# Kernel tuning notes

Measured on AMD Instinct MI355X. Metric: run time of the kernel, lower is better.

Reference implementation:

```python
import jax, jax.numpy as jnp
import numpy as np

CONTEXT_SIZE = 2048
CONTEXT_DIM = 1024
HIDDEN_SIZE = 1024
BATCH = 32
SEQLEN = 64


def setup_inputs() -> dict:
    key = jax.random.key(0)
    k1, k2, k3 = jax.random.split(key, 3)
    hidden = jax.random.normal(k1, (1, BATCH, HIDDEN_SIZE), dtype=jnp.float32)
    contextvects = jax.random.normal(k2, (CONTEXT_SIZE, BATCH, CONTEXT_DIM), dtype=jnp.float32)
    # nn.Linear weight: [out_features=context_dim, in_features=hidden_size]
    W = jax.random.normal(k3, (CONTEXT_DIM, HIDDEN_SIZE), dtype=jnp.float32) / np.sqrt(HIDDEN_SIZE)
    padding_mask = jnp.zeros((CONTEXT_SIZE, BATCH), dtype=bool)
    return {"seqlen": SEQLEN, "hidden": hidden, "contextvects": contextvects,
            "W": W, "padding_mask": padding_mask}


def reference(seqlen, hidden, contextvects, W, padding_mask):
    # hidden: [1, B, H] -> [B, H]
    h = hidden[0]
    # Linear projection (no bias): [B, D]
    hidden_proj = h @ W.T
    # scores over context positions: [C, B]
    scores = jnp.einsum('cbd,bd->cb', contextvects, hidden_proj)
    scores = jnp.where(padding_mask, -jnp.inf, scores)
    # softmax over context dim (dim=0)
    attn_weights = jax.nn.softmax(scores, axis=0)  # [C, B]
    # weighted sum of context vectors: [B, D]
    ctx = jnp.einsum('cb,cbd->bd', attn_weights, contextvects)
    # the torch loop recomputes identical values for every step -> broadcast
    context = jnp.broadcast_to(ctx[None], (seqlen, ctx.shape[0], ctx.shape[1]))
    attentions = jnp.broadcast_to(attn_weights.T[None],
                                  (seqlen, attn_weights.shape[1], attn_weights.shape[0]))
    return context, attentions
```

## Files before the change

kernel.cpp:

```cpp
#include <hip/hip_runtime.h>
#include <math.h>

#define C_SIZE 2048
#define D_DIM  1024
#define H_DIM  1024
#define B_SIZE 32
#define S_LEN  64
#define G_NUM  32
#define CG     (C_SIZE / G_NUM)

__global__ __launch_bounds__(256) void hp_kernel(const float* __restrict__ hidden,
                                                 const float* __restrict__ W,
                                                 float* __restrict__ hp) {
    int b     = blockIdx.x;
    int dbase = blockIdx.y * 128;
    int lane  = threadIdx.x & 63;
    int wave  = threadIdx.x >> 6;

    const float* hrow = hidden + b * H_DIM;
    float4 h4[4];
#pragma unroll
    for (int k = 0; k < 4; ++k) h4[k] = *(const float4*)(hrow + k * 256 + 4 * lane);

    for (int i = 0; i < 32; ++i) {
        int d = dbase + wave * 32 + i;
        const float* wrow = W + (size_t)d * H_DIM;
        float s = 0.f;
#pragma unroll
        for (int k = 0; k < 4; ++k) {
            float4 w4 = *(const float4*)(wrow + k * 256 + 4 * lane);
            s += w4.x * h4[k].x + w4.y * h4[k].y + w4.z * h4[k].z + w4.w * h4[k].w;
        }
        for (int off = 32; off > 0; off >>= 1) s += __shfl_xor(s, off);
        if (lane == 0) hp[b * D_DIM + d] = s;
    }
}

__global__ __launch_bounds__(256) void fused_kernel(const float* __restrict__ cv,
                                                    const float* __restrict__ hp,
                                                    const unsigned char* __restrict__ mask,
                                                    float* __restrict__ scoresT,
                                                    float* __restrict__ pm,
                                                    float* __restrict__ pl,
                                                    float* __restrict__ pacc) {
    int g    = blockIdx.x;
    int b    = blockIdx.y;
    int lane = threadIdx.x & 63;
    int wave = threadIdx.x >> 6;

    const float* hpb = hp + b * D_DIM;
    float4 hp4[4];
#pragma unroll
    for (int k = 0; k < 4; ++k) hp4[k] = *(const float4*)(hpb + k * 256 + 4 * lane);

    float  m = -3.0e38f, l = 0.f;
    float4 acc[4];
#pragma unroll
    for (int k = 0; k < 4; ++k) acc[k] = make_float4(0.f, 0.f, 0.f, 0.f);

    const int    c0      = g * CG + wave * (CG / 4);
    const size_t cstride = (size_t)B_SIZE * D_DIM;
    const float* p0      = cv + ((size_t)c0 * B_SIZE + b) * D_DIM + 4 * lane;

    float4 nxt[4];
#pragma unroll
    for (int k = 0; k < 4; ++k) nxt[k] = *(const float4*)(p0 + k * 256);

    for (int i = 0; i < 16; ++i) {
        float4 cvv[4];
#pragma unroll
        for (int k = 0; k < 4; ++k) cvv[k] = nxt[k];
        if (i < 15) {
            const float* pn = p0 + (size_t)(i + 1) * cstride;
#pragma unroll
            for (int k = 0; k < 4; ++k) nxt[k] = *(const float4*)(pn + k * 256);
        }
        float s = 0.f;
#pragma unroll
        for (int k = 0; k < 4; ++k) {
            s += cvv[k].x * hp4[k].x + cvv[k].y * hp4[k].y +
                 cvv[k].z * hp4[k].z + cvv[k].w * hp4[k].w;
        }
        for (int off = 32; off > 0; off >>= 1) s += __shfl_xor(s, off);

        int c = c0 + i;
        if (mask[c * B_SIZE + b]) s = -3.0e38f;
        if (lane == 0) scoresT[b * C_SIZE + c] = s;

        if (s <= m) {
            float p = __expf(s - m);
            l += p;
#pragma unroll
            for (int k = 0; k < 4; ++k) {
                acc[k].x += p * cvv[k].x;
                acc[k].y += p * cvv[k].y;
                acc[k].z += p * cvv[k].z;
                acc[k].w += p * cvv[k].w;
            }
        } else {
            float scale = __expf(m - s);
            l = l * scale + 1.f;
#pragma unroll
            for (int k = 0; k < 4; ++k) {
                acc[k].x = acc[k].x * scale + cvv[k].x;
                acc[k].y = acc[k].y * scale + cvv[k].y;
                acc[k].z = acc[k].z * scale + cvv[k].z;
                acc[k].w = acc[k].w * scale + cvv[k].w;
            }
            m = s;
        }
    }

    __shared__ float sm[4], sl[4];
    __shared__ float accs[4][D_DIM];
    if (lane == 0) { sm[wave] = m; sl[wave] = l; }
    __syncthreads();

    float mb = fmaxf(fmaxf(sm[0], sm[1]), fmaxf(sm[2], sm[3]));
    float myscale = __expf(m - mb);
#pragma unroll
    for (int k = 0; k < 4; ++k) {
        float4 v = acc[k];
        v.x *= myscale; v.y *= myscale; v.z *= myscale; v.w *= myscale;
        *(float4*)&accs[wave][k * 256 + 4 * lane] = v;
    }
    float lb = 0.f;
#pragma unroll
    for (int w = 0; w < 4; ++w) lb += sl[w] * __expf(sm[w] - mb);
    __syncthreads();

    int t = threadIdx.x;
    float4 r = make_float4(0.f, 0.f, 0.f, 0.f);
#pragma unroll
    for (int w = 0; w < 4; ++w) {
        float4 v = *(const float4*)&accs[w][t * 4];
        r.x += v.x; r.y += v.y; r.z += v.z; r.w += v.w;
    }
    *(float4*)(pacc + ((size_t)g * B_SIZE + b) * D_DIM + t * 4) = r;
    if (t == 0) { pm[g * B_SIZE + b] = mb; pl[g * B_SIZE + b] = lb; }
}

__global__ __launch_bounds__(64) void ctx_kernel(const float* __restrict__ pm,
                                                 const float* __restrict__ pl,
                                                 const float* __restrict__ pacc,
                                                 float* __restrict__ Mb,
                                                 float* __restrict__ Lb,
                                                 float* __restrict__ ctxws) {
    int b     = blockIdx.x;
    int dbase = blockIdx.y * 256;
    int lane  = threadIdx.x;

    float mg = (lane < G_NUM) ? pm[lane * B_SIZE + b] : -3.0e38f;
    float M = mg;
    for (int off = 32; off > 0; off >>= 1) M = fmaxf(M, __shfl_xor(M, off));
    float lg = (lane < G_NUM) ? pl[lane * B_SIZE + b] * __expf(mg - M) : 0.f;
    float L = lg;
    for (int off = 32; off > 0; off >>= 1) L += __shfl_xor(L, off);

    __shared__ float ssc[G_NUM];
    if (lane < G_NUM) ssc[lane] = __expf(mg - M);
    __syncthreads();

    float4 r = make_float4(0.f, 0.f, 0.f, 0.f);
#pragma unroll 8
    for (int gi = 0; gi < G_NUM; ++gi) {
        float sc = ssc[gi];
        float4 v = *(const float4*)(pacc + ((size_t)gi * B_SIZE + b) * D_DIM + dbase + 4 * lane);
        r.x += sc * v.x; r.y += sc * v.y; r.z += sc * v.z; r.w += sc * v.w;
    }
    float invL = 1.f / L;
    r.x *= invL; r.y *= invL; r.z *= invL; r.w *= invL;
    *(float4*)(ctxws + b * D_DIM + dbase + 4 * lane) = r;

    if (blockIdx.y == 0 && lane == 0) { Mb[b] = M; Lb[b] = L; }
}

__global__ __launch_bounds__(256) void out_kernel(const float* __restrict__ ctxws,
                                                  const float* __restrict__ scoresT,
                                                  const float* __restrict__ Mb,
                                                  const float* __restrict__ Lb,
                                                  float* __restrict__ out_ctx,
                                                  float* __restrict__ out_attn) {
    int blk = blockIdx.x;
    int b   = blk & (B_SIZE - 1);
    int t   = threadIdx.x;

    float4 cx = *(const float4*)(ctxws + b * D_DIM + t * 4);
    *(float4*)(out_ctx + (size_t)blk * D_DIM + t * 4) = cx;

    float M    = Mb[b];
    float invL = 1.f / Lb[b];
    const float* srow = scoresT + b * C_SIZE;
    float4* orow = (float4*)(out_attn + (size_t)blk * C_SIZE);
#pragma unroll
    for (int k = 0; k < 2; ++k) {
        int c4 = t + k * 256;
        float4 sv = *(const float4*)(srow + c4 * 4);
        float4 av;
        av.x = __expf(sv.x - M) * invL;
        av.y = __expf(sv.y - M) * invL;
        av.z = __expf(sv.z - M) * invL;
        av.w = __expf(sv.w - M) * invL;
        orow[c4] = av;
    }
}

extern "C" void kernel_launch(void* const* d_in, const int* in_sizes, int n_in,
                              void* d_out, int out_size, void* d_ws, size_t ws_size,
                              hipStream_t stream) {
    const float*         hidden = (const float*)d_in[1];
    const float*         cv     = (const float*)d_in[2];
    const float*         W      = (const float*)d_in[3];
    const unsigned char* mask   = (const unsigned char*)d_in[4];

    float* ws = (float*)d_ws;
    float* hp      = ws;
    float* scoresT = ws + 32768;
    float* pm      = ws + 98304;
    float* pl      = ws + 99328;
    float* Mb      = ws + 100352;
    float* Lb      = ws + 100384;
    float* ctxws   = ws + 100416;
    float* pacc    = ws + 133184;

    float* out_ctx  = (float*)d_out;
    float* out_attn = (float*)d_out + (size_t)S_LEN * B_SIZE * D_DIM;

    hp_kernel<<<dim3(B_SIZE, 8), 256, 0, stream>>>(hidden, W, hp);
    fused_kernel<<<dim3(G_NUM, B_SIZE), 256, 0, stream>>>(cv, hp, mask, scoresT, pm, pl, pacc);
    ctx_kernel<<<dim3(B_SIZE, 4), 64, 0, stream>>>(pm, pl, pacc, Mb, Lb, ctxws);
    out_kernel<<<dim3(S_LEN * B_SIZE), 256, 0, stream>>>(ctxws, scoresT, Mb, Lb, out_ctx, out_attn);
}
```

Measured before the change: 77.13 us.

## Merge four kernels into one persistent kernel with atomic grid barriers

Replaces the four separate launches (projection, fused score/softmax/accumulate, context reduce, output broadcast) with a single 512-block kernel. Stages are separated by software grid barriers built on agent-scope atomics, with the counters cleared by a memset before launch. The context split drops from 32 to 16 groups, each wave covering 32 positions, and the W loads in the projection stage are double-buffered. This removes launch gaps and inter-kernel drain, but needs all 512 blocks resident at once for the barrier to work and adds spin-wait overhead.

```diff
diff --git a/kernel.cpp b/kernel.cpp
--- a/kernel.cpp
+++ b/kernel.cpp
@@ -6,202 +6,237 @@
 #define H_DIM  1024
 #define B_SIZE 32
 #define S_LEN  64
-#define G_NUM  32
-#define CG     (C_SIZE / G_NUM)
-
-__global__ __launch_bounds__(256) void hp_kernel(const float* __restrict__ hidden,
-                                                 const float* __restrict__ W,
-                                                 float* __restrict__ hp) {
-    int b     = blockIdx.x;
-    int dbase = blockIdx.y * 128;
-    int lane  = threadIdx.x & 63;
-    int wave  = threadIdx.x >> 6;
-
-    const float* hrow = hidden + b * H_DIM;
-    float4 h4[4];
-#pragma unroll
-    for (int k = 0; k < 4; ++k) h4[k] = *(const float4*)(hrow + k * 256 + 4 * lane);
-
-    for (int i = 0; i < 32; ++i) {
-        int d = dbase + wave * 32 + i;
-        const float* wrow = W + (size_t)d * H_DIM;
-        float s = 0.f;
+#define G_NUM  16
+#define NBLK   512
+
+__device__ __forceinline__ void grid_barrier(unsigned* cnt, int tid) {
+    __syncthreads();
+    if (tid == 0) {
+        __hip_atomic_fetch_add(cnt, 1u, __ATOMIC_RELEASE, __HIP_MEMORY_SCOPE_AGENT);
+        for (int i = 0; i < (1 << 22); ++i) {
+            if (__hip_atomic_load(cnt, __ATOMIC_ACQUIRE, __HIP_MEMORY_SCOPE_AGENT) >= NBLK)
+                break;
+            __builtin_amdgcn_s_sleep(2);
+        }
+    }
+    __syncthreads();
+}
+
+__global__ __launch_bounds__(256, 2) void mega_kernel(
+    const float* __restrict__ hidden,
+    const float* __restrict__ W,
+    const float* __restrict__ cv,
+    const unsigned char* __restrict__ mask,
+    float* __restrict__ out_ctx,
+    float* __restrict__ out_attn,
+    float* __restrict__ ws)
+{
+    unsigned* bar0 = (unsigned*)ws;
+    unsigned* bar1 = (unsigned*)ws + 16;
+    unsigned* bar2 = (unsigned*)ws + 32;
+    float* hp      = ws + 64;
+    float* scoresT = ws + 32832;
+    float* pm      = ws + 98368;
+    float* pl      = ws + 98880;
+    float* Mb      = ws + 99392;
+    float* Lb      = ws + 99424;
+    float* ctxws   = ws + 99456;
+    float* pacc    = ws + 132224;
+
+    const int bid  = blockIdx.x;
+    const int tid  = threadIdx.x;
+    const int lane = tid & 63;
+    const int wave = tid >> 6;
+
+    __shared__ float accs[4][D_DIM];
+    __shared__ float sm[4], sl[4];
+    __shared__ float ssc[G_NUM];
+
+    {
+        const int dg = bid >> 5;
+        const int b  = bid & 31;
+        const float* hrow = hidden + b * H_DIM;
+        float4 h4[4];
+#pragma unroll
+        for (int k = 0; k < 4; ++k) h4[k] = *(const float4*)(hrow + k * 256 + 4 * lane);
+
+        const int d0 = dg * 64 + wave * 16;
+        const float* wp = W + (size_t)d0 * H_DIM + 4 * lane;
+        float4 wb[2][4];
+#pragma unroll
+        for (int k = 0; k < 4; ++k) wb[0][k] = *(const float4*)(wp + k * 256);
+
+#pragma unroll
+        for (int i = 0; i < 16; ++i) {
+            if (i < 15) {
+                const float* wn = wp + (size_t)(i + 1) * H_DIM;
+#pragma unroll
+                for (int k = 0; k < 4; ++k) wb[(i + 1) & 1][k] = *(const float4*)(wn + k * 256);
+            }
+            float s = 0.f;
+#pragma unroll
+            for (int k = 0; k < 4; ++k) {
+                float4 w4 = wb[i & 1][k];
+                s += w4.x * h4[k].x + w4.y * h4[k].y + w4.z * h4[k].z + w4.w * h4[k].w;
+            }
+            for (int off = 32; off > 0; off >>= 1) s += __shfl_xor(s, off);
+            if (lane == 0) hp[b * D_DIM + d0 + i] = s;
+        }
+    }
+
+    grid_barrier(bar0, tid);
+
+    {
+        const int g = bid >> 5;
+        const int b = bid & 31;
+
+        const float* hpb = hp + b * D_DIM;
+        float4 hp4[4];
+#pragma unroll
+        for (int k = 0; k < 4; ++k) hp4[k] = *(const float4*)(hpb + k * 256 + 4 * lane);
+
+        float  m = -3.0e38f, l = 0.f;
+        float4 acc[4];
+#pragma unroll
+        for (int k = 0; k < 4; ++k) acc[k] = make_float4(0.f, 0.f, 0.f, 0.f);
+
+        const int    c0      = g * 128 + wave * 32;
+        const size_t cstride = (size_t)B_SIZE * D_DIM;
+        const float* p0      = cv + ((size_t)c0 * B_SIZE + b) * D_DIM + 4 * lane;
+
+        float4 nxt[4];
+#pragma unroll
+        for (int k = 0; k < 4; ++k) nxt[k] = *(const float4*)(p0 + k * 256);
+
+        for (int i = 0; i < 32; ++i) {
+            float4 cvv[4];
+#pragma unroll
+            for (int k = 0; k < 4; ++k) cvv[k] = nxt[k];
+            if (i < 31) {
+                const float* pn = p0 + (size_t)(i + 1) * cstride;
+#pragma unroll
+                for (int k = 0; k < 4; ++k) nxt[k] = *(const float4*)(pn + k * 256);
+            }
+            float s = 0.f;
+#pragma unroll
+            for (int k = 0; k < 4; ++k) {
+                s += cvv[k].x * hp4[k].x + cvv[k].y * hp4[k].y +
+                     cvv[k].z * hp4[k].z + cvv[k].w * hp4[k].w;
+            }
+            for (int off = 32; off > 0; off >>= 1) s += __shfl_xor(s, off);
+
+            int c = c0 + i;
+            if (mask[c * B_SIZE + b]) s = -3.0e38f;
+            if (lane == 0) scoresT[b * C_SIZE + c] = s;
+
+            if (s <= m) {
+                float p = __expf(s - m);
+                l += p;
+#pragma unroll
+                for (int k = 0; k < 4; ++k) {
+                    acc[k].x += p * cvv[k].x;
+                    acc[k].y += p * cvv[k].y;
+                    acc[k].z += p * cvv[k].z;
+                    acc[k].w += p * cvv[k].w;
+                }
+            } else {
+                float scale = __expf(m - s);
+                l = l * scale + 1.f;
+#pragma unroll
+                for (int k = 0; k < 4; ++k) {
+                    acc[k].x = acc[k].x * scale + cvv[k].x;
+                    acc[k].y = acc[k].y * scale + cvv[k].y;
+                    acc[k].z = acc[k].z * scale + cvv[k].z;
+                    acc[k].w = acc[k].w * scale + cvv[k].w;
+                }
+                m = s;
+            }
+        }
+
+        if (lane == 0) { sm[wave] = m; sl[wave] = l; }
+        __syncthreads();
+
+        float mb = fmaxf(fmaxf(sm[0], sm[1]), fmaxf(sm[2], sm[3]));
+        float myscale = __expf(m - mb);
 #pragma unroll
         for (int k = 0; k < 4; ++k) {
-            float4 w4 = *(const float4*)(wrow + k * 256 + 4 * lane);
-            s += w4.x * h4[k].x + w4.y * h4[k].y + w4.z * h4[k].z + w4.w * h4[k].w;
-        }
-        for (int off = 32; off > 0; off >>= 1) s += __shfl_xor(s, off);
-        if (lane == 0) hp[b * D_DIM + d] = s;
-    }
-}
-
-__global__ __launch_bounds__(256) void fused_kernel(const float* __restrict__ cv,
-                                                    const float* __restrict__ hp,
-                                                    const unsigned char* __restrict__ mask,
-                                                    float* __restrict__ scoresT,
-                                                    float* __restrict__ pm,
-                                                    float* __restrict__ pl,
-                                                    float* __restrict__ pacc) {
-    int g    = blockIdx.x;
-    int b    = blockIdx.y;
-    int lane = threadIdx.x & 63;
-    int wave = threadIdx.x >> 6;
-
-    const float* hpb = hp + b * D_DIM;
-    float4 hp4[4];
-#pragma unroll
-    for (int k = 0; k < 4; ++k) hp4[k] = *(const float4*)(hpb + k * 256 + 4 * lane);
-
-    float  m = -3.0e38f, l = 0.f;
-    float4 acc[4];
-#pragma unroll
-    for (int k = 0; k < 4; ++k) acc[k] = make_float4(0.f, 0.f, 0.f, 0.f);
-
-    const int    c0      = g * CG + wave * (CG / 4);
-    const size_t cstride = (size_t)B_SIZE * D_DIM;
-    const float* p0      = cv + ((size_t)c0 * B_SIZE + b) * D_DIM + 4 * lane;
-
-    float4 nxt[4];
-#pragma unroll
-    for (int k = 0; k < 4; ++k) nxt[k] = *(const float4*)(p0 + k * 256);
-
-    for (int i = 0; i < 16; ++i) {
-        float4 cvv[4];
-#pragma unroll
-        for (int k = 0; k < 4; ++k) cvv[k] = nxt[k];
-        if (i < 15) {
-            const float* pn = p0 + (size_t)(i + 1) * cstride;
-#pragma unroll
-            for (int k = 0; k < 4; ++k) nxt[k] = *(const float4*)(pn + k * 256);
-        }
-        float s = 0.f;
-#pragma unroll
-        for (int k = 0; k < 4; ++k) {
-            s += cvv[k].x * hp4[k].x + cvv[k].y * hp4[k].y +
-                 cvv[k].z * hp4[k].z + cvv[k].w * hp4[k].w;
-        }
-        for (int off = 32; off > 0; off >>= 1) s += __shfl_xor(s, off);
-
-        int c = c0 + i;
-        if (mask[c * B_SIZE + b]) s = -3.0e38f;
-        if (lane == 0) scoresT[b * C_SIZE + c] = s;
-
-        if (s <= m) {
-            float p = __expf(s - m);
-            l += p;
-#pragma unroll
-            for (int k = 0; k < 4; ++k) {
-                acc[k].x += p * cvv[k].x;
-                acc[k].y += p * cvv[k].y;
-                acc[k].z += p * cvv[k].z;
-                acc[k].w += p * cvv[k].w;
-            }
-        } else {
-            float scale = __expf(m - s);
-            l = l * scale + 1.f;
-#pragma unroll
-            for (int k = 0; k < 4; ++k) {
-                acc[k].x = acc[k].x * scale + cvv[k].x;
-                acc[k].y = acc[k].y * scale + cvv[k].y;
-                acc[k].z = acc[k].z * scale + cvv[k].z;
-                acc[k].w = acc[k].w * scale + cvv[k].w;
-            }
-            m = s;
-        }
-    }
-
-    __shared__ float sm[4], sl[4];
-    __shared__ float accs[4][D_DIM];
-    if (lane == 0) { sm[wave] = m; sl[wave] = l; }
-    __syncthreads();
-
-    float mb = fmaxf(fmaxf(sm[0], sm[1]), fmaxf(sm[2], sm[3]));
-    float myscale = __expf(m - mb);
-#pragma unroll
-    for (int k = 0; k < 4; ++k) {
-        float4 v = acc[k];
-        v.x *= myscale; v.y *= myscale; v.z *= myscale; v.w *= myscale;
-        *(float4*)&accs[wave][k * 256 + 4 * lane] = v;
-    }
-    float lb = 0.f;
-#pragma unroll
-    for (int w = 0; w < 4; ++w) lb += sl[w] * __expf(sm[w] - mb);
-    __syncthreads();
-
-    int t = threadIdx.x;
-    float4 r = make_float4(0.f, 0.f, 0.f, 0.f);
-#pragma unroll
-    for (int w = 0; w < 4; ++w) {
-        float4 v = *(const float4*)&accs[w][t * 4];
-        r.x += v.x; r.y += v.y; r.z += v.z; r.w += v.w;
-    }
-    *(float4*)(pacc + ((size_t)g * B_SIZE + b) * D_DIM + t * 4) = r;
-    if (t == 0) { pm[g * B_SIZE + b] = mb; pl[g * B_SIZE + b] = lb; }
-}
-
-__global__ __launch_bounds__(64) void ctx_kernel(const float* __restrict__ pm,
-                                                 const float* __restrict__ pl,
-                                                 const float* __restrict__ pacc,
-                                                 float* __restrict__ Mb,
-                                                 float* __restrict__ Lb,
-                                                 float* __restrict__ ctxws) {
-    int b     = blockIdx.x;
-    int dbase = blockIdx.y * 256;
-    int lane  = threadIdx.x;
-
-    float mg = (lane < G_NUM) ? pm[lane * B_SIZE + b] : -3.0e38f;
-    float M = mg;
-    for (int off = 32; off > 0; off >>= 1) M = fmaxf(M, __shfl_xor(M, off));
-    float lg = (lane < G_NUM) ? pl[lane * B_SIZE + b] * __expf(mg - M) : 0.f;
-    float L = lg;
-    for (int off = 32; off > 0; off >>= 1) L += __shfl_xor(L, off);
-
-    __shared__ float ssc[G_NUM];
-    if (lane < G_NUM) ssc[lane] = __expf(mg - M);
-    __syncthreads();
-
-    float4 r = make_float4(0.f, 0.f, 0.f, 0.f);
-#pragma unroll 8
-    for (int gi = 0; gi < G_NUM; ++gi) {
-        float sc = ssc[gi];
-        float4 v = *(const float4*)(pacc + ((size_t)gi * B_SIZE + b) * D_DIM + dbase + 4 * lane);
-        r.x += sc * v.x; r.y += sc * v.y; r.z += sc * v.z; r.w += sc * v.w;
-    }
-    float invL = 1.f / L;
-    r.x *= invL; r.y *= invL; r.z *= invL; r.w *= invL;
-    *(float4*)(ctxws + b * D_DIM + dbase + 4 * lane) = r;
-
-    if (blockIdx.y == 0 && lane == 0) { Mb[b] = M; Lb[b] = L; }
-}
-
-__global__ __launch_bounds__(256) void out_kernel(const float* __restrict__ ctxws,
-                                                  const float* __restrict__ scoresT,
-                                                  const float* __restrict__ Mb,
-                                                  const float* __restrict__ Lb,
-                                                  float* __restrict__ out_ctx,
-                                                  float* __restrict__ out_attn) {
-    int blk = blockIdx.x;
-    int b   = blk & (B_SIZE - 1);
-    int t   = threadIdx.x;
-
-    float4 cx = *(const float4*)(ctxws + b * D_DIM + t * 4);
-    *(float4*)(out_ctx + (size_t)blk * D_DIM + t * 4) = cx;
-
-    float M    = Mb[b];
-    float invL = 1.f / Lb[b];
-    const float* srow = scoresT + b * C_SIZE;
-    float4* orow = (float4*)(out_attn + (size_t)blk * C_SIZE);
-#pragma unroll
-    for (int k = 0; k < 2; ++k) {
-        int c4 = t + k * 256;
-        float4 sv = *(const float4*)(srow + c4 * 4);
-        float4 av;
-        av.x = __expf(sv.x - M) * invL;
-        av.y = __expf(sv.y - M) * invL;
-        av.z = __expf(sv.z - M) * invL;
-        av.w = __expf(sv.w - M) * invL;
-        orow[c4] = av;
+            float4 v = acc[k];
+            v.x *= myscale; v.y *= myscale; v.z *= myscale; v.w *= myscale;
+            *(float4*)&accs[wave][k * 256 + 4 * lane] = v;
+        }
+        float lb = 0.f;
+#pragma unroll
+        for (int w = 0; w < 4; ++w) lb += sl[w] * __expf(sm[w] - mb);
+        __syncthreads();
+
+        float4 r = make_float4(0.f, 0.f, 0.f, 0.f);
+#pragma unroll
+        for (int w = 0; w < 4; ++w) {
+            float4 v = *(const float4*)&accs[w][tid * 4];
+            r.x += v.x; r.y += v.y; r.z += v.z; r.w += v.w;
+        }
+        *(float4*)(pacc + ((size_t)g * B_SIZE + b) * D_DIM + tid * 4) = r;
+        if (tid == 0) { pm[g * B_SIZE + b] = mb; pl[g * B_SIZE + b] = lb; }
+    }
+
+    grid_barrier(bar1, tid);
+
+    if ((bid & 3) == 0) {
+        int k  = bid >> 2;
+        int b  = k >> 2;
+        int dq = k & 3;
+
+        float mg = (lane < G_NUM) ? pm[lane * B_SIZE + b] : -3.0e38f;
+        float M = mg;
+        for (int off = 32; off > 0; off >>= 1) M = fmaxf(M, __shfl_xor(M, off));
+        float lg = (lane < G_NUM) ? pl[lane * B_SIZE + b] * __expf(mg - M) : 0.f;
+        float L = lg;
+        for (int off = 32; off > 0; off >>= 1) L += __shfl_xor(L, off);
+
+        if (wave == 0 && lane < G_NUM) ssc[lane] = __expf(mg - M);
+        __syncthreads();
+
+        float invL = 1.f / L;
+        int d = dq * 256 + tid;
+        float r = 0.f;
+#pragma unroll
+        for (int gi = 0; gi < G_NUM; ++gi)
+            r += ssc[gi] * pacc[(size_t)(gi * B_SIZE + b) * D_DIM + d];
+        ctxws[b * D_DIM + d] = r * invL;
+
+        if ((k & 3) == 0 && tid == 0) { Mb[b] = M; Lb[b] = L; }
+    }
+
+    grid_barrier(bar2, tid);
+
+    {
+#pragma unroll
+        for (int j = 0; j < 4; ++j) {
+            int r = bid + j * NBLK;
+            int b = r & 31;
+            float4 v = *(const float4*)(ctxws + b * D_DIM + tid * 4);
+            *(float4*)(out_ctx + (size_t)r * D_DIM + tid * 4) = v;
+        }
+#pragma unroll
+        for (int j = 0; j < 4; ++j) {
+            int r = bid + j * NBLK;
+            int b = r & 31;
+            float M    = Mb[b];
+            float invL = 1.f / Lb[b];
+            const float* srow = scoresT + b * C_SIZE;
+            float4* orow = (float4*)(out_attn + (size_t)r * C_SIZE);
+#pragma unroll
+            for (int kk = 0; kk < 2; ++kk) {
+                int c4 = tid + kk * 256;
+                float4 sv = *(const float4*)(srow + c4 * 4);
+                float4 av;
+                av.x = __expf(sv.x - M) * invL;
+                av.y = __expf(sv.y - M) * invL;
+                av.z = __expf(sv.z - M) * invL;
+                av.w = __expf(sv.w - M) * invL;
+                orow[c4] = av;
+            }
+        }
     }
 }
 
@@ -213,21 +248,12 @@
     const float*         W      = (const float*)d_in[3];
     const unsigned char* mask   = (const unsigned char*)d_in[4];
 
-    float* ws = (float*)d_ws;
-    float* hp      = ws;
-    float* scoresT = ws + 32768;
-    float* pm      = ws + 98304;
-    float* pl      = ws + 99328;
-    float* Mb      = ws + 100352;
-    float* Lb      = ws + 100384;
-    float* ctxws   = ws + 100416;
-    float* pacc    = ws + 133184;
-
     float* out_ctx  = (float*)d_out;
     float* out_attn = (float*)d_out + (size_t)S_LEN * B_SIZE * D_DIM;
-
-    hp_kernel<<<dim3(B_SIZE, 8), 256, 0, stream>>>(hidden, W, hp);
-    fused_kernel<<<dim3(G_NUM, B_SIZE), 256, 0, stream>>>(cv, hp, mask, scoresT, pm, pl, pacc);
-    ctx_kernel<<<dim3(B_SIZE, 4), 64, 0, stream>>>(pm, pl, pacc, Mb, Lb, ctxws);
-    out_kernel<<<dim3(S_LEN * B_SIZE), 256, 0, stream>>>(ctxws, scoresT, Mb, Lb, out_ctx, out_attn);
+    float* wsp      = (float*)d_ws;
+
+    hipMemsetAsync(d_ws, 0, 256, stream);
+
+    mega_kernel<<<dim3(NBLK), dim3(256), 0, stream>>>(hidden, W, cv, mask,
+                                                      out_ctx, out_attn, wsp);
 }
```

New measurement: 206.7 us. +168.0%, slower.
